# Kernel tuning notes

Hardware: AMD Instinct MI355X
Metric: run time of the kernel (lower is better)

Reference implementation:

```python
import jax, jax.numpy as jnp
import numpy as np

B, NQ, NKV = 4, 1024, 2048
Q_DIM = K_DIM = V_DIM = 1024
HEADS, DIM_HEAD = 16, 64
INNER = HEADS * DIM_HEAD


def setup_inputs() -> dict:
    key = jax.random.key(0)
    ks = jax.random.split(key, 10)
    return {
        "x": jax.random.normal(ks[0], (B, NQ, Q_DIM), dtype=jnp.float32),
        "key_t": jax.random.normal(ks[1], (B, NKV, K_DIM), dtype=jnp.float32),
        "value": jax.random.normal(ks[2], (B, NKV, V_DIM), dtype=jnp.float32),
        "mask": jax.random.randint(ks[3], (B, NQ, NKV), 0, 2) == 1,
        "Wq": jax.random.normal(ks[4], (Q_DIM, INNER), dtype=jnp.float32) * (Q_DIM ** -0.5),
        "Wk": jax.random.normal(ks[5], (K_DIM, INNER), dtype=jnp.float32) * (K_DIM ** -0.5),
        "Wv": jax.random.normal(ks[6], (V_DIM, INNER), dtype=jnp.float32) * (V_DIM ** -0.5),
        "Wo": jax.random.normal(ks[7], (INNER, Q_DIM), dtype=jnp.float32) * (INNER ** -0.5),
        "gamma": jnp.ones((Q_DIM,), dtype=jnp.float32),
        "beta": jnp.zeros((Q_DIM,), dtype=jnp.float32),
    }


def reference(x, key_t, value, mask, Wq, Wk, Wv, Wo, gamma, beta):
    # LayerNorm over last dim
    mu = jnp.mean(x, axis=-1, keepdims=True)
    var = jnp.var(x, axis=-1, keepdims=True)
    xn = (x - mu) * jax.lax.rsqrt(var + 1e-5) * gamma + beta

    h, d = HEADS, DIM_HEAD
    # b n (h d) -> b h n d
    q = (xn @ Wq).reshape(B, NQ, h, d).transpose(0, 2, 1, 3)
    k = (key_t @ Wk).reshape(B, NKV, h, d).transpose(0, 2, 1, 3)
    v = (value @ Wv).reshape(B, NKV, h, d).transpose(0, 2, 1, 3)

    scale = d ** -0.5
    dots = jnp.einsum("bhnd,bhmd->bhnm", q, k) * scale  # [b,h,nq,nkv]
    min_neg = -jnp.finfo(dots.dtype).max
    dots = jnp.where(mask[:, None, :, :], min_neg, dots)
    attn = jax.nn.softmax(dots, axis=-1)
    out = jnp.einsum("bhnm,bhmd->bhnd", attn, v)
    out = out.transpose(0, 2, 1, 3).reshape(B, NQ, INNER)  # b h n d -> b n (h d)
    return out @ Wo
```

## Files before the change

### kernel.cpp

```cpp
#include <hip/hip_runtime.h>

typedef unsigned short u16;
typedef unsigned int u32;
typedef unsigned char u8;

typedef __attribute__((ext_vector_type(8))) short bf16x8;
typedef __attribute__((ext_vector_type(4))) short bf16x4;
typedef __attribute__((ext_vector_type(4))) float f32x4;

__device__ __forceinline__ float bf2f(u16 u) {
    union { u32 i; float f; } v; v.i = ((u32)u) << 16; return v.f;
}
__device__ __forceinline__ u16 f2bf(float f) {
    union { float f; u32 i; } v; v.f = f;
    u32 r = v.i + 0x7fffu + ((v.i >> 16) & 1u);
    return (u16)(r >> 16);
}
__device__ __forceinline__ u32 pkbf(float a, float b) {
#if __has_builtin(__builtin_amdgcn_cvt_pk_bf16_f32)
    auto r = __builtin_amdgcn_cvt_pk_bf16_f32(a, b);
    u32 u; __builtin_memcpy(&u, &r, 4); return u;
#else
    return (u32)f2bf(a) | ((u32)f2bf(b) << 16);
#endif
}

__device__ __forceinline__ void async16(u16* lds, const u16* g) {
    __builtin_amdgcn_global_load_lds(
        (const __attribute__((address_space(1))) void*)g,
        (__attribute__((address_space(3))) void*)lds, 16, 0, 0);
}

__global__ __launch_bounds__(256) void detect_dtype(const u32* __restrict__ x,
                                                    int* __restrict__ flag) {
    int tid = threadIdx.x;
    int hits = 0;
    for (int i = 0; i < 4; ++i) {
        u32 w = x[tid * 4 + i];
        u32 e = (w >> 7) & 0xFFu;
        hits += (e >= 110u && e <= 131u) ? 1 : 0;
    }
    for (int off = 1; off < 64; off <<= 1) hits += __shfl_xor(hits, off, 64);
    __shared__ int red[4];
    int wave = tid >> 6, lane = tid & 63;
    if (lane == 0) red[wave] = hits;
    __syncthreads();
    if (tid == 0) flag[0] = (red[0] + red[1] + red[2] + red[3] > 512) ? 1 : 0;
}

__global__ __launch_bounds__(256) void conv_bf16(const void* __restrict__ src,
                                                 u16* __restrict__ dst,
                                                 const int* __restrict__ flagp) {
    int flag = *flagp;
    size_t i = (size_t)blockIdx.x * 256 + threadIdx.x;
    if (flag) {
        ((uint4*)dst)[i] = ((const uint4*)src)[i];
    } else {
        const float4* s = (const float4*)src + i * 2;
        float4 f0 = s[0], f1 = s[1];
        u16 t[8];
        t[0] = f2bf(f0.x); t[1] = f2bf(f0.y); t[2] = f2bf(f0.z); t[3] = f2bf(f0.w);
        t[4] = f2bf(f1.x); t[5] = f2bf(f1.y); t[6] = f2bf(f1.z); t[7] = f2bf(f1.w);
        ((uint4*)dst)[i] = *(const uint4*)t;
    }
}

__global__ __launch_bounds__(256) void mask_pack(const int* __restrict__ m,
                                                 u8* __restrict__ o) {
    size_t i = (size_t)blockIdx.x * 256 + threadIdx.x;
    const int4* mp = (const int4*)m + i * 4;
    uint4 out;
    u32* op = (u32*)&out;
    for (int j = 0; j < 4; ++j) {
        int4 a = mp[j];
        op[j] = (a.x == 0 ? 0xFFu : 0u) | (a.y == 0 ? 0xFF00u : 0u) |
                (a.z == 0 ? 0xFF0000u : 0u) | (a.w == 0 ? 0xFF000000u : 0u);
    }
    ((uint4*)o)[i] = out;
}

__global__ __launch_bounds__(256) void ln_kernel(const void* __restrict__ x_,
                                                 const void* __restrict__ g_,
                                                 const void* __restrict__ b_,
                                                 u16* __restrict__ out,
                                                 const int* __restrict__ flagp) {
    int flag = *flagp;
    int row = blockIdx.x;
    int tid = threadIdx.x;
    float v[4];
    if (flag) {
        const u16* xr = (const u16*)x_ + (size_t)row * 1024;
        uint2 d = *(const uint2*)&xr[tid * 4];
        v[0] = bf2f((u16)(d.x & 0xffff));
        v[1] = bf2f((u16)(d.x >> 16));
        v[2] = bf2f((u16)(d.y & 0xffff));
        v[3] = bf2f((u16)(d.y >> 16));
    } else {
        const float* xr = (const float*)x_ + (size_t)row * 1024;
        float4 d = *(const float4*)&xr[tid * 4];
        v[0] = d.x; v[1] = d.y; v[2] = d.z; v[3] = d.w;
    }
    float s  = v[0] + v[1] + v[2] + v[3];
    float ss = v[0]*v[0] + v[1]*v[1] + v[2]*v[2] + v[3]*v[3];
    for (int off = 1; off < 64; off <<= 1) {
        s  += __shfl_xor(s,  off, 64);
        ss += __shfl_xor(ss, off, 64);
    }
    __shared__ float red[8];
    int wave = tid >> 6, lane = tid & 63;
    if (lane == 0) { red[wave] = s; red[4 + wave] = ss; }
    __syncthreads();
    s  = red[0] + red[1] + red[2] + red[3];
    ss = red[4] + red[5] + red[6] + red[7];
    float mu   = s * (1.0f / 1024.0f);
    float var  = ss * (1.0f / 1024.0f) - mu * mu;
    float rstd = rsqrtf(var + 1e-5f);
    u16 r01[4];
    for (int j = 0; j < 4; ++j) {
        float g, bb;
        if (flag) { g = bf2f(((const u16*)g_)[tid * 4 + j]); bb = bf2f(((const u16*)b_)[tid * 4 + j]); }
        else      { g = ((const float*)g_)[tid * 4 + j];     bb = ((const float*)b_)[tid * 4 + j]; }
        r01[j] = f2bf((v[j] - mu) * rstd * g + bb);
    }
    uint2 o;
    o.x = (u32)r01[0] | ((u32)r01[1] << 16);
    o.y = (u32)r01[2] | ((u32)r01[3] << 16);
    *(uint2*)&out[(size_t)row * 1024 + tid * 4] = o;
}

__global__ __launch_bounds__(256) void transpose64(const void* __restrict__ src_,
                                                   u16* __restrict__ dst,
                                                   int rows, int cols,
                                                   const int* __restrict__ flagp) {
    __shared__ u16 t[64][65];
    int flag = *flagp;
    int bx = blockIdx.x * 64;
    int by = blockIdx.y * 64;
    int tid = threadIdx.x;
    for (int i = 0; i < 16; ++i) {
        int r = i * 4 + (tid >> 6);
        int c = tid & 63;
        size_t idx = (size_t)(by + r) * cols + bx + c;
        t[r][c] = flag ? ((const u16*)src_)[idx] : f2bf(((const float*)src_)[idx]);
    }
    __syncthreads();
    for (int i = 0; i < 16; ++i) {
        int r = i * 4 + (tid >> 6);
        int c = tid & 63;
        dst[(size_t)(bx + r) * rows + by + c] = t[c][r];
    }
}

__global__ __launch_bounds__(256, 2) void gemm128(const u16* __restrict__ A,
                                                  const u16* __restrict__ Bt,
                                                  void* __restrict__ C_,
                                                  int M, int N, int K,
                                                  const int* __restrict__ flagp,
                                                  int c_flagged, float cscale,
                                                  int vt_mode, int mdiv) {
    __shared__ u16 As[128 * 64];
    __shared__ u16 Bs[128 * 64];
    int flag = *flagp;
    bool c_bf16 = c_flagged ? (flag != 0) : true;

    int id  = blockIdx.x;
    int j   = id >> 3;
    int gy  = (id & 7) + 8 * (j % mdiv);
    int bnt = j / mdiv;

    int tid  = threadIdx.x;
    int wave = tid >> 6, lane = tid & 63;
    int quad = lane >> 4, l16 = lane & 15;
    size_t bm = (size_t)gy * 128;
    size_t bn = (size_t)bnt * 128;
    int wm = (wave >> 1) * 64, wn = (wave & 1) * 64;

    int lr  = lane >> 3;
    int csw = (lane & 7) ^ lr;
    const u16* Ag = A  + (bm + wave * 32 + lr) * (size_t)K + csw * 8;
    const u16* Bg = Bt + (bn + wave * 32 + lr) * (size_t)K + csw * 8;
    u16* Al = &As[(wave * 32) * 64];
    u16* Bl = &Bs[(wave * 32) * 64];

    f32x4 acc[4][4];
#pragma unroll
    for (int i = 0; i < 4; ++i)
#pragma unroll
        for (int jj = 0; jj < 4; ++jj)
            acc[i][jj] = (f32x4){0.f, 0.f, 0.f, 0.f};

    int rsw = l16 & 7;

    for (int k0 = 0; k0 < K; k0 += 64) {
        __syncthreads();
#pragma unroll
        for (int i = 0; i < 4; ++i) {
            async16(Al + i * 8 * 64, Ag + (size_t)i * 8 * K + k0);
            async16(Bl + i * 8 * 64, Bg + (size_t)i * 8 * K + k0);
        }
        __syncthreads();

#pragma unroll
        for (int ks = 0; ks < 2; ++ks) {
            int chunk = ((ks << 2) | quad) ^ rsw;
            bf16x8 af[4], bfr[4];
#pragma unroll
            for (int mi = 0; mi < 4; ++mi)
                af[mi]  = *(const bf16x8*)&As[(wm + mi * 16 + l16) * 64 + chunk * 8];
#pragma unroll
            for (int ni = 0; ni < 4; ++ni)
                bfr[ni] = *(const bf16x8*)&Bs[(wn + ni * 16 + l16) * 64 + chunk * 8];
#pragma unroll
            for (int mi = 0; mi < 4; ++mi)
#pragma unroll
                for (int ni = 0; ni < 4; ++ni)
                    acc[mi][ni] = __builtin_amdgcn_mfma_f32_16x16x32_bf16(
                        af[mi], bfr[ni], acc[mi][ni], 0, 0, 0);
        }
    }

    if (vt_mode) {
        u16* C = (u16*)C_;
#pragma unroll
        for (int mi = 0; mi < 4; ++mi)
#pragma unroll
            for (int ni = 0; ni < 4; ++ni) {
                size_t m = bm + wm + mi * 16 + quad * 4;
                size_t n = bn + wn + ni * 16 + l16;
                size_t bb = m >> 11, kv = m & 2047;
                size_t hh = n >> 6,  d  = n & 63;
                u16 t4[4];
#pragma unroll
                for (int r = 0; r < 4; ++r) t4[r] = f2bf(acc[mi][ni][r]);
                *(uint2*)&C[((bb * 16 + hh) * 64 + d) * 2048 + kv] = *(const uint2*)t4;
            }
    } else {
#pragma unroll
        for (int mi = 0; mi < 4; ++mi)
#pragma unroll
            for (int ni = 0; ni < 4; ++ni)
#pragma unroll
                for (int r = 0; r < 4; ++r) {
                    size_t row = bm + wm + mi * 16 + quad * 4 + r;
                    size_t col = bn + wn + ni * 16 + l16;
                    float val = acc[mi][ni][r] * cscale;
                    if (c_bf16) ((u16*)C_)[row * N + col]   = f2bf(val);
                    else        ((float*)C_)[row * N + col] = val;
                }
    }
}

__global__ __launch_bounds__(256) void attn_kernel(const u16* __restrict__ qg,
                                                   const u16* __restrict__ kg,
                                                   const u16* __restrict__ vtg,
                                                   const u8* __restrict__ masku,
                                                   u16* __restrict__ og) {
    __shared__ u16 Ks[64 * 64];
    __shared__ u16 Vst[64 * 64];

    const int NQc = 1024, NKVc = 2048, HD = 1024;
    int id = blockIdx.x;
    int j  = id >> 3;
    int qt = j >> 3;
    int g  = (id & 7) + ((j & 7) << 3);
    int h  = g & 15;
    int b  = g >> 4;

    int tid  = threadIdx.x;
    int wave = tid >> 6, lane = tid & 63;
    int quad = lane >> 4, l16 = lane & 15;
    int q0 = qt * 64;

    const u16* qrow = qg + ((size_t)b * NQc + q0 + wave * 16 + l16) * HD + h * 64;
    bf16x8 aq0 = *(const bf16x8*)&qrow[quad * 8];
    bf16x8 aq1 = *(const bf16x8*)&qrow[32 + quad * 8];

    int lr  = lane >> 3;
    int csw = (lane & 7) ^ lr;
    const u16* kbase = kg  + ((size_t)b * NKVc + wave * 8 + lr) * HD + h * 64 + csw * 8;
    const u16* vbase = vtg + (((size_t)b * 16 + h) * 64 + wave * 8 + lr) * (size_t)NKVc + csw * 8;
    u16* kl = Ks  + (wave * 8) * 64;
    u16* vl = Vst + (wave * 8) * 64;

    f32x4 O[4], lacc;
#pragma unroll
    for (int dt = 0; dt < 4; ++dt) O[dt] = (f32x4){0.f, 0.f, 0.f, 0.f};
    lacc = (f32x4){0.f, 0.f, 0.f, 0.f};

    bf16x4 ones4;
#pragma unroll
    for (int jj = 0; jj < 4; ++jj) ones4[jj] = (short)0x3F80;

    const u8* mrow = masku + ((size_t)b * NQc + q0 + wave * 16 + l16) * (size_t)NKVc;

    int l7 = l16 & 7;

    for (int kv0 = 0; kv0 < NKVc; kv0 += 64) {
        __syncthreads();
#pragma unroll
        for (int i = 0; i < 2; ++i) {
            async16(kl + i * 32 * 64, kbase + ((size_t)kv0 + i * 32) * HD);
            async16(vl + i * 32 * 64, vbase + (size_t)(i * 32) * NKVc + kv0);
        }
        __syncthreads();

        bf16x4 pfr[4];
#pragma unroll
        for (int nt = 0; nt < 4; ++nt) {
            const u16* krow = Ks + (nt * 16 + l16) * 64;
            bf16x8 bk0 = *(const bf16x8*)&krow[(quad ^ l7) * 8];
            bf16x8 bk1 = *(const bf16x8*)&krow[((4 + quad) ^ l7) * 8];
            f32x4 st = (f32x4){0.f, 0.f, 0.f, 0.f};
            st = __builtin_amdgcn_mfma_f32_16x16x32_bf16(bk0, aq0, st, 0, 0, 0);
            st = __builtin_amdgcn_mfma_f32_16x16x32_bf16(bk1, aq1, st, 0, 0, 0);

            u32 mword = *(const u32*)&mrow[kv0 + nt * 16 + quad * 4];
            u32 p01 = pkbf(exp2f(st[0]), exp2f(st[1])) &
                      __builtin_amdgcn_perm(0u, mword, 0x01010000u);
            u32 p23 = pkbf(exp2f(st[2]), exp2f(st[3])) &
                      __builtin_amdgcn_perm(0u, mword, 0x03030202u);
            uint2 pu; pu.x = p01; pu.y = p23;
            pfr[nt] = *(const bf16x4*)&pu;

            lacc = __builtin_amdgcn_mfma_f32_16x16x16bf16_1k(ones4, pfr[nt], lacc, 0, 0, 0);
        }

#pragma unroll
        for (int dt = 0; dt < 4; ++dt) {
            const u16* vrow = Vst + (dt * 16 + l16) * 64;
#pragma unroll
            for (int kvs = 0; kvs < 4; ++kvs) {
                int gran = ((kvs << 1) | (quad >> 1)) ^ l7;
                bf16x4 av = *(const bf16x4*)&vrow[gran * 8 + (quad & 1) * 4];
                O[dt] = __builtin_amdgcn_mfma_f32_16x16x16bf16_1k(av, pfr[kvs], O[dt], 0, 0, 0);
            }
        }
    }

    float inv = 1.0f / lacc[0];
    u16* orow = og + ((size_t)b * NQc + q0 + wave * 16 + l16) * HD + h * 64;
#pragma unroll
    for (int dt = 0; dt < 4; ++dt) {
        u16 t4[4];
#pragma unroll
        for (int r = 0; r < 4; ++r) t4[r] = f2bf(O[dt][r] * inv);
        *(uint2*)&orow[dt * 16 + quad * 4] = *(const uint2*)t4;
    }
}

extern "C" void kernel_launch(void* const* d_in, const int* in_sizes, int n_in,
                              void* d_out, int out_size, void* d_ws, size_t ws_size,
                              hipStream_t stream) {
    const void* x     = d_in[0];
    const void* key   = d_in[1];
    const void* value = d_in[2];
    const int*  mask  = (const int*)d_in[3];
    const void* Wq    = d_in[4];
    const void* Wk    = d_in[5];
    const void* Wv    = d_in[6];
    const void* Wo    = d_in[7];
    const void* gamma = d_in[8];
    const void* beta  = d_in[9];

    char* ws = (char*)d_ws;
    int* flag = (int*)(ws);
    u16* xn  = (u16*)(ws + ( 1ull << 20));
    u8*  mu8 = (u8*) (ws + ( 1ull << 20));
    u16* q   = (u16*)(ws + ( 9ull << 20));
    u16* kb  = (u16*)(ws + ( 9ull << 20));
    u16* ao  = (u16*)(ws + (17ull << 20));
    u16* k   = (u16*)(ws + (25ull << 20));
    u16* vb  = (u16*)(ws + (25ull << 20));
    u16* vT  = (u16*)(ws + (41ull << 20));
    u16* Wqt = (u16*)(ws + (57ull << 20));
    u16* Wkt = (u16*)(ws + (59ull << 20));
    u16* Wvt = (u16*)(ws + (61ull << 20));
    u16* Wot = (u16*)(ws + (63ull << 20));

    const float QSCALE = 0.125f * 1.44269504f;

    detect_dtype<<<1, 256, 0, stream>>>((const u32*)x, flag);

    ln_kernel<<<4096, 256, 0, stream>>>(x, gamma, beta, xn, flag);

    dim3 tg(16, 16);
    transpose64<<<tg, 256, 0, stream>>>(Wq, Wqt, 1024, 1024, flag);
    transpose64<<<tg, 256, 0, stream>>>(Wk, Wkt, 1024, 1024, flag);
    transpose64<<<tg, 256, 0, stream>>>(Wv, Wvt, 1024, 1024, flag);
    transpose64<<<tg, 256, 0, stream>>>(Wo, Wot, 1024, 1024, flag);

    conv_bf16<<<4096, 256, 0, stream>>>(key,   kb, flag);
    conv_bf16<<<4096, 256, 0, stream>>>(value, vb, flag);

    gemm128<<<512, 256, 0, stream>>>(vb, Wvt, vT, 8192, 1024, 1024, flag, 0, 1.0f, 1, 8);
    gemm128<<<512, 256, 0, stream>>>(kb, Wkt, k,  8192, 1024, 1024, flag, 0, 1.0f, 0, 8);
    gemm128<<<256, 256, 0, stream>>>(xn, Wqt, q,  4096, 1024, 1024, flag, 0, QSCALE, 0, 4);

    mask_pack<<<2048, 256, 0, stream>>>(mask, mu8);

    attn_kernel<<<1024, 256, 0, stream>>>(q, k, vT, mu8, ao);

    gemm128<<<256, 256, 0, stream>>>(ao, Wot, d_out, 4096, 1024, 1024, flag, 1, 1.0f, 0, 4);
}
```

Measured before the change: 396.9 us.

## Double-buffer K/V tiles in attention kernel to overlap loads with MFMA

```diff
diff --git a/kernel.cpp b/kernel.cpp
--- a/kernel.cpp
+++ b/kernel.cpp
@@ -255,8 +255,8 @@
                                                    const u16* __restrict__ vtg,
                                                    const u8* __restrict__ masku,
                                                    u16* __restrict__ og) {
-    __shared__ u16 Ks[64 * 64];
-    __shared__ u16 Vst[64 * 64];
+    __shared__ u16 Ks[2 * 64 * 64];
+    __shared__ u16 Vst[2 * 64 * 64];
 
     const int NQc = 1024, NKVc = 2048, HD = 1024;
     int id = blockIdx.x;
@@ -279,8 +279,6 @@
     int csw = (lane & 7) ^ lr;
     const u16* kbase = kg  + ((size_t)b * NKVc + wave * 8 + lr) * HD + h * 64 + csw * 8;
     const u16* vbase = vtg + (((size_t)b * 16 + h) * 64 + wave * 8 + lr) * (size_t)NKVc + csw * 8;
-    u16* kl = Ks  + (wave * 8) * 64;
-    u16* vl = Vst + (wave * 8) * 64;
 
     f32x4 O[4], lacc;
 #pragma unroll
@@ -295,19 +293,37 @@
 
     int l7 = l16 & 7;
 
+    {
+        u16* kl = Ks  + (wave * 8) * 64;
+        u16* vl = Vst + (wave * 8) * 64;
+#pragma unroll
+        for (int i = 0; i < 2; ++i) {
+            async16(kl + i * 32 * 64, kbase + (size_t)(i * 32) * HD);
+            async16(vl + i * 32 * 64, vbase + (size_t)(i * 32) * NKVc);
+        }
+    }
+    asm volatile("s_waitcnt vmcnt(0)" ::: "memory");
+    __builtin_amdgcn_s_barrier();
+
+    int cur = 0;
     for (int kv0 = 0; kv0 < NKVc; kv0 += 64) {
-        __syncthreads();
-#pragma unroll
-        for (int i = 0; i < 2; ++i) {
-            async16(kl + i * 32 * 64, kbase + ((size_t)kv0 + i * 32) * HD);
-            async16(vl + i * 32 * 64, vbase + (size_t)(i * 32) * NKVc + kv0);
-        }
-        __syncthreads();
+        if (kv0 + 64 < NKVc) {
+            u16* kl = Ks  + (cur ^ 1) * 4096 + (wave * 8) * 64;
+            u16* vl = Vst + (cur ^ 1) * 4096 + (wave * 8) * 64;
+#pragma unroll
+            for (int i = 0; i < 2; ++i) {
+                async16(kl + i * 32 * 64, kbase + ((size_t)kv0 + 64 + i * 32) * HD);
+                async16(vl + i * 32 * 64, vbase + (size_t)(i * 32) * NKVc + kv0 + 64);
+            }
+        }
+
+        const u16* Kb = Ks  + cur * 4096;
+        const u16* Vb = Vst + cur * 4096;
 
         bf16x4 pfr[4];
 #pragma unroll
         for (int nt = 0; nt < 4; ++nt) {
-            const u16* krow = Ks + (nt * 16 + l16) * 64;
+            const u16* krow = Kb + (nt * 16 + l16) * 64;
             bf16x8 bk0 = *(const bf16x8*)&krow[(quad ^ l7) * 8];
             bf16x8 bk1 = *(const bf16x8*)&krow[((4 + quad) ^ l7) * 8];
             f32x4 st = (f32x4){0.f, 0.f, 0.f, 0.f};
@@ -327,7 +343,7 @@
 
 #pragma unroll
         for (int dt = 0; dt < 4; ++dt) {
-            const u16* vrow = Vst + (dt * 16 + l16) * 64;
+            const u16* vrow = Vb + (dt * 16 + l16) * 64;
 #pragma unroll
             for (int kvs = 0; kvs < 4; ++kvs) {
                 int gran = ((kvs << 1) | (quad >> 1)) ^ l7;
@@ -335,6 +351,10 @@
                 O[dt] = __builtin_amdgcn_mfma_f32_16x16x16bf16_1k(av, pfr[kvs], O[dt], 0, 0, 0);
             }
         }
+
+        asm volatile("s_waitcnt vmcnt(0)" ::: "memory");
+        __builtin_amdgcn_s_barrier();
+        cur ^= 1;
     }
 
     float inv = 1.0f / lacc[0];
```

Measured after the change: 396.2 us. About the same (-0.2%).
